# Kernel tuning notes

Measured on AMD Instinct MI355X. Metric: run time of the kernel, lower is better.

## Reference

```python
import jax, jax.numpy as jnp
import numpy as np

EPS = 1e-07
B, N = 128, 512


def setup_inputs() -> dict:
    key = jax.random.key(0)
    k1, k2, k3 = jax.random.split(key, 3)
    pred = jax.random.normal(k1, (B, N), dtype=jnp.float32)
    target = jax.random.uniform(k2, (B, N), dtype=jnp.float32)  # survival times in (0,1)
    valid_mask = jax.random.bernoulli(k3, p=0.9, shape=(B, N))  # bool
    return {"pred": pred, "target": target, "valid_mask": valid_mask}


def reference(pred, target, valid_mask):
    # pred, target: (B, N) float32; valid_mask: (B, N) bool
    n = pred.shape[1]
    target_masked = jnp.where(valid_mask, target, jnp.float32(-1.0))  # (B, N)
    T_i = target_masked[:, :, None]  # (B, N, 1)
    T_j = target_masked[:, None, :]  # (B, 1, N)
    batch_max_time = jnp.max(target_masked, axis=1, keepdims=True)[:, :, None]  # (B, 1, 1)

    # player i is eliminated (not the final survivor) and valid
    is_elimination = (T_i < batch_max_time) & (T_i > 0) & valid_mask[:, :, None]  # (B, N, 1)
    # risk set at time t_i: players j still alive (T_j >= T_i) and valid
    risk_set_mask = (T_j >= T_i) & valid_mask[:, None, :]  # (B, N, N)

    pred_j = pred[:, None, :]  # (B, 1, N)
    risk_pred_masked = jnp.where(risk_set_mask, pred_j, -jnp.inf)  # (B, N, N)
    log_denominator = jax.nn.logsumexp(risk_pred_masked, axis=2, keepdims=True)  # (B, N, 1)
    log_probs = pred_j - log_denominator  # (B, N, N)

    # part 1: -log p of the eliminated player itself (diagonal)
    log_prob_eliminated = jnp.diagonal(log_probs, axis1=1, axis2=2)[:, :, None]  # (B, N, 1)
    loss_part1 = -log_prob_eliminated * is_elimination

    # part 2: -log(1 - p_i) for survivors i in risk set (excluding eliminated)
    probs = jnp.exp(log_probs)
    eye = jnp.eye(n, dtype=bool)[None]  # (1, N, N)
    surviving_mask = risk_set_mask & ~eye
    probs_clamped = jnp.minimum(probs, 1.0 - EPS)
    loss_surviving = -jnp.log(1.0 - probs_clamped + EPS)
    loss_part2 = jnp.sum(loss_surviving * surviving_mask.astype(pred.dtype), axis=2, keepdims=True)
    loss_part2 = loss_part2 * is_elimination

    total_loss_per_batch = jnp.sum(loss_part1 + loss_part2, axis=1)  # (B, 1)
    valid_batch_mask = (jnp.sum(valid_mask, axis=1) >= 2).astype(pred.dtype)  # (B,)
    final_loss = jnp.sum(jnp.squeeze(total_loss_per_batch, axis=1) * valid_batch_mask)
    num_valid = jnp.maximum(jnp.sum(valid_batch_mask), 1.0)
    return final_loss / num_valid
```

## Files before the change

### kernel.cpp

```cpp
#include <hip/hip_runtime.h>
#include <math.h>

#define BB 128
#define NN 512
#define CHUNKS 8
#define RPB (NN / CHUNKS)
#define RPW (RPB / 4)
#define GRID (BB * CHUNKS)
#define EPSF 1e-7f
#define ONEP (1.0f + EPSF)
#define TWOEPS (2.0f * EPSF)

__global__ __launch_bounds__(256) void cox_main(const float* __restrict__ pred,
                                                const float* __restrict__ target,
                                                const int* __restrict__ valid,
                                                float* __restrict__ ws) {
    __shared__ float s_e[NN];
    __shared__ float s_tm[NN];
    __shared__ float s_max[4];
    __shared__ float s_cnt[4];
    __shared__ float s_acc[4];

    const int b     = blockIdx.x / CHUNKS;
    const int chunk = blockIdx.x % CHUNKS;
    const int tid   = threadIdx.x;
    const int lane  = tid & 63;
    const int wave  = tid >> 6;

    float lmax = -1.0f, lcnt = 0.0f;
    #pragma unroll
    for (int k = 0; k < NN / 256; ++k) {
        int j = tid + 256 * k;
        float p = pred[b * NN + j];
        float t = target[b * NN + j];
        int   v = valid[b * NN + j];
        float tm = v ? t : -1.0f;
        s_e[j]  = __expf(p);
        s_tm[j] = tm;
        lmax = fmaxf(lmax, tm);
        lcnt += v ? 1.0f : 0.0f;
    }
    #pragma unroll
    for (int off = 32; off; off >>= 1) {
        lmax = fmaxf(lmax, __shfl_xor(lmax, off, 64));
        lcnt += __shfl_xor(lcnt, off, 64);
    }
    if (lane == 0) { s_max[wave] = lmax; s_cnt[wave] = lcnt; }
    __syncthreads();
    const float bmax = fmaxf(fmaxf(s_max[0], s_max[1]), fmaxf(s_max[2], s_max[3]));
    const float bcnt = s_cnt[0] + s_cnt[1] + s_cnt[2] + s_cnt[3];
    const float batch_valid = (bcnt >= 2.0f) ? 1.0f : 0.0f;

    float tj[8], e0[8];
    #pragma unroll
    for (int k = 0; k < 8; ++k) {
        tj[k] = s_tm[lane + 64 * k];
        e0[k] = s_e[lane + 64 * k];
    }

    float acc = 0.0f;
    const int row0 = chunk * RPB + wave * RPW;
    for (int r0 = 0; r0 < RPW; r0 += 2) {
        float Ti[2], ei[2], elim[2], S[2], prod[2];
        float em[2][8];
        #pragma unroll
        for (int rr = 0; rr < 2; ++rr) {
            const int i = row0 + r0 + rr;
            float t = s_tm[i];
            bool el = (t > 0.0f && t < bmax);
            elim[rr] = el ? 1.0f : 0.0f;
            Ti[rr]   = el ? t : INFINITY;
            ei[rr]   = s_e[i];
            S[rr]    = 0.0f;
            prod[rr] = 1.0f;
        }
        #pragma unroll
        for (int k = 0; k < 8; ++k) {
            #pragma unroll
            for (int rr = 0; rr < 2; ++rr) {
                float x = (tj[k] >= Ti[rr]) ? e0[k] : 0.0f;
                em[rr][k] = x;
                S[rr] += x;
            }
        }
        #pragma unroll
        for (int off = 32; off; off >>= 1) {
            #pragma unroll
            for (int rr = 0; rr < 2; ++rr)
                S[rr] += __shfl_xor(S[rr], off, 64);
        }
        float invS[2], F[2];
        #pragma unroll
        for (int rr = 0; rr < 2; ++rr) {
            float Sc = (elim[rr] != 0.0f) ? S[rr] : 1.0f;
            float is = __builtin_amdgcn_rcpf(Sc);
            invS[rr] = is;
            float qii = fmaxf(fmaf(-ei[rr], is, ONEP), TWOEPS);
            F[rr] = is * ei[rr] * __builtin_amdgcn_rcpf(qii);
        }
        #pragma unroll
        for (int k = 0; k < 8; ++k) {
            #pragma unroll
            for (int rr = 0; rr < 2; ++rr)
                prod[rr] *= fmaxf(fmaf(-em[rr][k], invS[rr], ONEP), TWOEPS);
        }
        #pragma unroll
        for (int rr = 0; rr < 2; ++rr) {
            const int i = row0 + r0 + rr;
            float mul = (lane == (i & 63)) ? F[rr] : 1.0f;
            prod[rr] *= mul;
            acc -= elim[rr] * __logf(prod[rr]);
        }
    }

    #pragma unroll
    for (int off = 32; off; off >>= 1) acc += __shfl_xor(acc, off, 64);
    if (lane == 0) s_acc[wave] = acc;
    __syncthreads();
    if (tid == 0) {
        ws[blockIdx.x] = (s_acc[0] + s_acc[1] + s_acc[2] + s_acc[3]) * batch_valid;
        if (chunk == 0) ws[GRID + b] = batch_valid;
    }
}

__global__ __launch_bounds__(256) void cox_final(const float* __restrict__ ws,
                                                 float* __restrict__ out) {
    __shared__ float s_tot[4];
    __shared__ float s_cnt[4];
    const int tid  = threadIdx.x;
    const int lane = tid & 63;
    const int wave = tid >> 6;

    float tot = 0.0f;
    #pragma unroll
    for (int k = 0; k < GRID / 256; ++k) tot += ws[tid + 256 * k];
    float cnt = (tid < BB) ? ws[GRID + tid] : 0.0f;

    #pragma unroll
    for (int off = 32; off; off >>= 1) {
        tot += __shfl_xor(tot, off, 64);
        cnt += __shfl_xor(cnt, off, 64);
    }
    if (lane == 0) { s_tot[wave] = tot; s_cnt[wave] = cnt; }
    __syncthreads();
    if (tid == 0) {
        float T = s_tot[0] + s_tot[1] + s_tot[2] + s_tot[3];
        float C = s_cnt[0] + s_cnt[1] + s_cnt[2] + s_cnt[3];
        out[0] = T / fmaxf(C, 1.0f);
    }
}

extern "C" void kernel_launch(void* const* d_in, const int* in_sizes, int n_in,
                              void* d_out, int out_size, void* d_ws, size_t ws_size,
                              hipStream_t stream) {
    const float* pred   = (const float*)d_in[0];
    const float* target = (const float*)d_in[1];
    const int*   valid  = (const int*)d_in[2];
    float* out = (float*)d_out;
    float* ws  = (float*)d_ws;

    cox_main<<<GRID, 256, 0, stream>>>(pred, target, valid, ws);
    cox_final<<<1, 256, 0, stream>>>(ws, out);
}
```

Measured before the change: 68.32 us.

## Map rows to lanes and split columns across eight waves

Restructures the main kernel so each lane owns one row i and each of eight waves handles a 64-column slice of j. Row sums are combined through shared memory instead of per-row wave shuffles, and the column data is read as broadcast float4 LDS loads. This removes the serial per-row loop and its shuffle reductions. In exchange it adds 64 registers of em per thread, two extra block barriers, and a 512-thread block.

Result: faster. 65.26 us (-4.5%).

```diff
diff --git a/kernel.cpp b/kernel.cpp
--- a/kernel.cpp
+++ b/kernel.cpp
@@ -4,22 +4,25 @@
 #define BB 128
 #define NN 512
 #define CHUNKS 8
-#define RPB (NN / CHUNKS)
-#define RPW (RPB / 4)
+#define RPB 64
+#define NWAVES 8
+#define NT (NWAVES * 64)
+#define JPW (NN / NWAVES)
 #define GRID (BB * CHUNKS)
 #define EPSF 1e-7f
 #define ONEP (1.0f + EPSF)
 #define TWOEPS (2.0f * EPSF)
 
-__global__ __launch_bounds__(256) void cox_main(const float* __restrict__ pred,
-                                                const float* __restrict__ target,
-                                                const int* __restrict__ valid,
-                                                float* __restrict__ ws) {
-    __shared__ float s_e[NN];
-    __shared__ float s_tm[NN];
-    __shared__ float s_max[4];
-    __shared__ float s_cnt[4];
-    __shared__ float s_acc[4];
+__global__ __launch_bounds__(NT) void cox_main(const float* __restrict__ pred,
+                                               const float* __restrict__ target,
+                                               const int* __restrict__ valid,
+                                               float* __restrict__ ws) {
+    __shared__ __align__(16) float s_e[NN];
+    __shared__ __align__(16) float s_tm[NN];
+    __shared__ float s_mx[NWAVES];
+    __shared__ float s_ct[NWAVES];
+    __shared__ float s_S[NWAVES][RPB];
+    __shared__ float s_L[NWAVES][RPB];
 
     const int b     = blockIdx.x / CHUNKS;
     const int chunk = blockIdx.x % CHUNKS;
@@ -27,99 +30,87 @@
     const int lane  = tid & 63;
     const int wave  = tid >> 6;
 
-    float lmax = -1.0f, lcnt = 0.0f;
+    {
+        float p = pred[b * NN + tid];
+        float t = target[b * NN + tid];
+        int   v = valid[b * NN + tid];
+        float tm = v ? t : -1.0f;
+        s_e[tid]  = __expf(p);
+        s_tm[tid] = tm;
+        float lmax = tm;
+        float lcnt = v ? 1.0f : 0.0f;
+        #pragma unroll
+        for (int off = 32; off; off >>= 1) {
+            lmax = fmaxf(lmax, __shfl_xor(lmax, off, 64));
+            lcnt += __shfl_xor(lcnt, off, 64);
+        }
+        if (lane == 0) { s_mx[wave] = lmax; s_ct[wave] = lcnt; }
+    }
+    __syncthreads();
+
+    float bmax = s_mx[0], bcnt = s_ct[0];
     #pragma unroll
-    for (int k = 0; k < NN / 256; ++k) {
-        int j = tid + 256 * k;
-        float p = pred[b * NN + j];
-        float t = target[b * NN + j];
-        int   v = valid[b * NN + j];
-        float tm = v ? t : -1.0f;
-        s_e[j]  = __expf(p);
-        s_tm[j] = tm;
-        lmax = fmaxf(lmax, tm);
-        lcnt += v ? 1.0f : 0.0f;
+    for (int w = 1; w < NWAVES; ++w) {
+        bmax = fmaxf(bmax, s_mx[w]);
+        bcnt += s_ct[w];
     }
-    #pragma unroll
-    for (int off = 32; off; off >>= 1) {
-        lmax = fmaxf(lmax, __shfl_xor(lmax, off, 64));
-        lcnt += __shfl_xor(lcnt, off, 64);
-    }
-    if (lane == 0) { s_max[wave] = lmax; s_cnt[wave] = lcnt; }
-    __syncthreads();
-    const float bmax = fmaxf(fmaxf(s_max[0], s_max[1]), fmaxf(s_max[2], s_max[3]));
-    const float bcnt = s_cnt[0] + s_cnt[1] + s_cnt[2] + s_cnt[3];
     const float batch_valid = (bcnt >= 2.0f) ? 1.0f : 0.0f;
 
-    float tj[8], e0[8];
+    const int   row    = chunk * RPB + lane;
+    const float ti_raw = s_tm[row];
+    const float ei     = s_e[row];
+    const bool  el     = (ti_raw > 0.0f) && (ti_raw < bmax);
+    const float elim   = el ? 1.0f : 0.0f;
+    const float Ti     = el ? ti_raw : INFINITY;
+
+    const int jb = wave * JPW;
+    float em[JPW];
+    float S0 = 0.0f, S1 = 0.0f, S2 = 0.0f, S3 = 0.0f;
     #pragma unroll
-    for (int k = 0; k < 8; ++k) {
-        tj[k] = s_tm[lane + 64 * k];
-        e0[k] = s_e[lane + 64 * k];
+    for (int k = 0; k < JPW; k += 4) {
+        const float4 t4 = *(const float4*)&s_tm[jb + k];
+        const float4 e4 = *(const float4*)&s_e[jb + k];
+        em[k + 0] = (t4.x >= Ti) ? e4.x : 0.0f; S0 += em[k + 0];
+        em[k + 1] = (t4.y >= Ti) ? e4.y : 0.0f; S1 += em[k + 1];
+        em[k + 2] = (t4.z >= Ti) ? e4.z : 0.0f; S2 += em[k + 2];
+        em[k + 3] = (t4.w >= Ti) ? e4.w : 0.0f; S3 += em[k + 3];
     }
+    s_S[wave][lane] = (S0 + S1) + (S2 + S3);
+    __syncthreads();
 
-    float acc = 0.0f;
-    const int row0 = chunk * RPB + wave * RPW;
-    for (int r0 = 0; r0 < RPW; r0 += 2) {
-        float Ti[2], ei[2], elim[2], S[2], prod[2];
-        float em[2][8];
+    float S = s_S[0][lane];
+    #pragma unroll
+    for (int w = 1; w < NWAVES; ++w) S += s_S[w][lane];
+    const float Sc   = el ? S : 1.0f;
+    const float invS = __builtin_amdgcn_rcpf(Sc);
+
+    float P0 = 1.0f, P1 = 1.0f, P2 = 1.0f, P3 = 1.0f;
+    #pragma unroll
+    for (int k = 0; k < JPW; k += 4) {
+        P0 *= fmaxf(fmaf(-em[k + 0], invS, ONEP), TWOEPS);
+        P1 *= fmaxf(fmaf(-em[k + 1], invS, ONEP), TWOEPS);
+        P2 *= fmaxf(fmaf(-em[k + 2], invS, ONEP), TWOEPS);
+        P3 *= fmaxf(fmaf(-em[k + 3], invS, ONEP), TWOEPS);
+    }
+    float P = (P0 * P1) * (P2 * P3);
+    if (wave == 0) {
+        const float qii = fmaxf(fmaf(-ei, invS, ONEP), TWOEPS);
+        P *= ei * invS * __builtin_amdgcn_rcpf(qii);
+    }
+    s_L[wave][lane] = __logf(P);
+    __syncthreads();
+
+    if (wave == 0) {
+        float lsum = s_L[0][lane];
         #pragma unroll
-        for (int rr = 0; rr < 2; ++rr) {
-            const int i = row0 + r0 + rr;
-            float t = s_tm[i];
-            bool el = (t > 0.0f && t < bmax);
-            elim[rr] = el ? 1.0f : 0.0f;
-            Ti[rr]   = el ? t : INFINITY;
-            ei[rr]   = s_e[i];
-            S[rr]    = 0.0f;
-            prod[rr] = 1.0f;
+        for (int w = 1; w < NWAVES; ++w) lsum += s_L[w][lane];
+        float acc = -elim * lsum;
+        #pragma unroll
+        for (int off = 32; off; off >>= 1) acc += __shfl_xor(acc, off, 64);
+        if (lane == 0) {
+            ws[blockIdx.x] = acc * batch_valid;
+            if (chunk == 0) ws[GRID + b] = batch_valid;
         }
-        #pragma unroll
-        for (int k = 0; k < 8; ++k) {
-            #pragma unroll
-            for (int rr = 0; rr < 2; ++rr) {
-                float x = (tj[k] >= Ti[rr]) ? e0[k] : 0.0f;
-                em[rr][k] = x;
-                S[rr] += x;
-            }
-        }
-        #pragma unroll
-        for (int off = 32; off; off >>= 1) {
-            #pragma unroll
-            for (int rr = 0; rr < 2; ++rr)
-                S[rr] += __shfl_xor(S[rr], off, 64);
-        }
-        float invS[2], F[2];
-        #pragma unroll
-        for (int rr = 0; rr < 2; ++rr) {
-            float Sc = (elim[rr] != 0.0f) ? S[rr] : 1.0f;
-            float is = __builtin_amdgcn_rcpf(Sc);
-            invS[rr] = is;
-            float qii = fmaxf(fmaf(-ei[rr], is, ONEP), TWOEPS);
-            F[rr] = is * ei[rr] * __builtin_amdgcn_rcpf(qii);
-        }
-        #pragma unroll
-        for (int k = 0; k < 8; ++k) {
-            #pragma unroll
-            for (int rr = 0; rr < 2; ++rr)
-                prod[rr] *= fmaxf(fmaf(-em[rr][k], invS[rr], ONEP), TWOEPS);
-        }
-        #pragma unroll
-        for (int rr = 0; rr < 2; ++rr) {
-            const int i = row0 + r0 + rr;
-            float mul = (lane == (i & 63)) ? F[rr] : 1.0f;
-            prod[rr] *= mul;
-            acc -= elim[rr] * __logf(prod[rr]);
-        }
-    }
-
-    #pragma unroll
-    for (int off = 32; off; off >>= 1) acc += __shfl_xor(acc, off, 64);
-    if (lane == 0) s_acc[wave] = acc;
-    __syncthreads();
-    if (tid == 0) {
-        ws[blockIdx.x] = (s_acc[0] + s_acc[1] + s_acc[2] + s_acc[3]) * batch_valid;
-        if (chunk == 0) ws[GRID + b] = batch_valid;
     }
 }
 
@@ -159,6 +150,6 @@
     float* out = (float*)d_out;
     float* ws  = (float*)d_ws;
 
-    cox_main<<<GRID, 256, 0, stream>>>(pred, target, valid, ws);
+    cox_main<<<GRID, NT, 0, stream>>>(pred, target, valid, ws);
     cox_final<<<1, 256, 0, stream>>>(ws, out);
 }
```
